# Performance work log

Hardware: AMD Instinct MI355X
Metric: run time of the kernel (lower is better)

The kernel has to match this reference:

```python
import jax, jax.numpy as jnp
import numpy as np

N = 50000
EPS = 1e-5


def gcn_conv(x, W, b, src, dst, n):
    # x: [n, Cin]; W: [Cin, Cout]; src/dst: [E+n] with self-loops included
    h = x @ W  # dense GEMM
    deg = jax.ops.segment_sum(jnp.ones_like(dst, dtype=h.dtype), dst, num_segments=n)
    dinv = jnp.where(deg > 0, jax.lax.rsqrt(deg), 0.0)
    norm = dinv[src] * dinv[dst]  # [E+n]
    msgs = h[src] * norm[:, None]  # gather + scale
    out = jax.ops.segment_sum(msgs, dst, num_segments=n)  # scatter-add
    return out + b


def batch_norm(x, gamma, beta, mean, var):
    return (x - mean) * jax.lax.rsqrt(var + EPS) * gamma + beta


def setup_inputs() -> dict:
    key = jax.random.key(0)
    ks = jax.random.split(key, 16)
    IN, H, OUT, E = 1280, 256, 500, 1600000
    x = jax.random.normal(ks[0], (N, IN), dtype=jnp.float32)
    edge_index = jax.random.randint(ks[1], (2, E), 0, N, dtype=jnp.int64)
    def lin(k, cin, cout):
        return jax.random.normal(k, (cin, cout), dtype=jnp.float32) / np.sqrt(cin)
    return {
        "x": x,
        "edge_index": edge_index,
        "W1": lin(ks[2], IN, H), "b1": jnp.zeros((H,), jnp.float32),
        "g1": jnp.ones((H,), jnp.float32), "be1": jnp.zeros((H,), jnp.float32),
        "m1": 0.1 * jax.random.normal(ks[3], (H,), jnp.float32),
        "v1": 0.5 + jax.random.uniform(ks[4], (H,), jnp.float32),
        "W2": lin(ks[5], H, H), "b2": jnp.zeros((H,), jnp.float32),
        "g2": jnp.ones((H,), jnp.float32), "be2": jnp.zeros((H,), jnp.float32),
        "m2": 0.1 * jax.random.normal(ks[6], (H,), jnp.float32),
        "v2": 0.5 + jax.random.uniform(ks[7], (H,), jnp.float32),
        "W3": lin(ks[8], H, OUT), "b3": jnp.zeros((OUT,), jnp.float32),
    }


def reference(x, edge_index, W1, b1, g1, be1, m1, v1, W2, b2, g2, be2, m2, v2, W3, b3):
    n = x.shape[0]
    loops = jnp.arange(n, dtype=edge_index.dtype)
    src = jnp.concatenate([edge_index[0], loops])
    dst = jnp.concatenate([edge_index[1], loops])
    h = gcn_conv(x, W1, b1, src, dst, n)
    h = jax.nn.relu(batch_norm(h, g1, be1, m1, v1))
    h = gcn_conv(h, W2, b2, src, dst, n)
    h = jax.nn.relu(batch_norm(h, g2, be2, m2, v2))
    return gcn_conv(h, W3, b3, src, dst, n)
```

## Files before the change

kernel.cpp:

```cpp
#include <hip/hip_runtime.h>
#include <hip/hip_bf16.h>
#include <stdint.h>

typedef __attribute__((ext_vector_type(4))) float f32x4;
typedef __attribute__((ext_vector_type(8))) short s16x8;
typedef __attribute__((ext_vector_type(4))) unsigned short u16x4;

#define EPSBN 1e-5f

__device__ __forceinline__ float bf2f(unsigned short u) {
  union { unsigned int i; float f; } w; w.i = ((unsigned int)u) << 16; return w.f;
}
__device__ __forceinline__ unsigned short f2bf(float f) {
  __hip_bfloat16 h = __float2bfloat16(f);
  unsigned short u; __builtin_memcpy(&u, &h, 2); return u;
}
__device__ __forceinline__ void gld_lds16(const unsigned short* g, unsigned short* l) {
  __builtin_amdgcn_global_load_lds(
      (__attribute__((address_space(1))) void*)(g),
      (__attribute__((address_space(3))) void*)(l), 16, 0, 0);
}

__global__ void k_init_deg(unsigned* deg, int n) {
  int i = blockIdx.x * 256 + threadIdx.x;
  if (i < n) deg[i] = 1u;
}
__global__ void k_count(const int* __restrict__ dst, unsigned* __restrict__ deg, int E) {
  int i = blockIdx.x * 256 + threadIdx.x;
  if (i < E) atomicAdd(&deg[dst[i]], 1u);
}
__global__ void k_dinv(const unsigned* __restrict__ deg, float* __restrict__ dinv, int n) {
  int i = blockIdx.x * 256 + threadIdx.x;
  if (i < n) dinv[i] = rsqrtf((float)deg[i]);
}
__global__ void k_bsum(const unsigned* __restrict__ deg, unsigned* __restrict__ bsum, int n) {
  __shared__ unsigned s[256];
  int t = threadIdx.x, i = blockIdx.x * 256 + t;
  s[t] = (i < n) ? deg[i] : 0u;
  __syncthreads();
  for (int st = 128; st > 0; st >>= 1) {
    if (t < st) s[t] += s[t + st];
    __syncthreads();
  }
  if (t == 0) bsum[blockIdx.x] = s[0];
}
__global__ void k_scan_top(const unsigned* __restrict__ bsum, unsigned* __restrict__ bpre,
                           int nb, unsigned* __restrict__ offs, int n) {
  __shared__ unsigned s[256];
  int t = threadIdx.x;
  unsigned v = (t < nb) ? bsum[t] : 0u;
  s[t] = v; __syncthreads();
  for (int d = 1; d < 256; d <<= 1) {
    unsigned a = (t >= d) ? s[t - d] : 0u;
    __syncthreads();
    s[t] += a;
    __syncthreads();
  }
  bpre[t] = s[t] - v;
  if (t == 255) offs[n] = s[255];
}
__global__ void k_scan_fin(const unsigned* __restrict__ deg, const unsigned* __restrict__ bpre,
                           unsigned* __restrict__ offs, unsigned* __restrict__ cur, int n) {
  __shared__ unsigned s[256];
  int t = threadIdx.x, i = blockIdx.x * 256 + t;
  unsigned v = (i < n) ? deg[i] : 0u;
  s[t] = v; __syncthreads();
  for (int d = 1; d < 256; d <<= 1) {
    unsigned a = (t >= d) ? s[t - d] : 0u;
    __syncthreads();
    s[t] += a;
    __syncthreads();
  }
  if (i < n) {
    unsigned o = bpre[blockIdx.x] + s[t] - v;
    offs[i] = o; cur[i] = o;
  }
}
__global__ void k_fill(const int* __restrict__ src, const int* __restrict__ dst,
                       unsigned* __restrict__ cur, int* __restrict__ adj, int E, int n) {
  int i = blockIdx.x * 256 + threadIdx.x;
  int s, d;
  if (i < E)          { s = src[i]; d = dst[i]; }
  else if (i < E + n) { s = d = i - E; }
  else return;
  unsigned p = atomicAdd(&cur[d], 1u);
  adj[p] = s;
}
#define SORT_CAP 96
__global__ __launch_bounds__(256) void k_sort(const unsigned* __restrict__ offs,
                                              int* __restrict__ adj, int nN) {
  __shared__ int buf[SORT_CAP * 256];
  int t = threadIdx.x;
  int v = blockIdx.x * 256 + t;
  if (v >= nN) return;
  unsigned b = offs[v], e = offs[v + 1];
  int len = (int)(e - b);
  if (len > SORT_CAP) return;
  for (int i = 0; i < len; ++i) buf[i * 256 + t] = adj[b + i];
  for (int i = 1; i < len; ++i) {
    int key = buf[i * 256 + t];
    int j = i - 1;
    while (j >= 0 && buf[j * 256 + t] > key) {
      buf[(j + 1) * 256 + t] = buf[j * 256 + t];
      --j;
    }
    buf[(j + 1) * 256 + t] = key;
  }
  for (int i = 0; i < len; ++i) adj[b + i] = buf[i * 256 + t];
}
__global__ __launch_bounds__(256) void k_edgew(const int* __restrict__ adj,
                                               const unsigned* __restrict__ offs,
                                               const float* __restrict__ dinv,
                                               int2* __restrict__ ew, int nN) {
  int wv = (blockIdx.x * 256 + threadIdx.x) >> 6;
  int lane = threadIdx.x & 63;
  if (wv >= nN) return;
  unsigned beg = offs[wv], end = offs[wv + 1];
  float dv = dinv[wv];
  for (unsigned e = beg + lane; e < end; e += 64) {
    int s = adj[e];
    ew[e] = make_int2(s, __float_as_int(dinv[s] * dv));
  }
}
__global__ void k_wt(const float* __restrict__ W, unsigned short* __restrict__ Wt,
                     int K, int N, int Npad) {
  int idx = blockIdx.x * 256 + threadIdx.x;
  if (idx >= Npad * K) return;
  int nn = idx / K, k = idx - nn * K;
  float v = (nn < N) ? W[(size_t)k * N + nn] : 0.f;
  Wt[idx] = f2bf(v);
}

#define BM 128
#define BN 128
#define BK 64

template<int CONVA, int OUTF32>
__global__ __launch_bounds__(256, 2) void k_gemm(
    const void* __restrict__ Aall, const unsigned short* __restrict__ Bt,
    void* __restrict__ Coutv, const float* __restrict__ bias,
    int M, int N, int K, int MT, int NT)
{
  __shared__ __align__(16) unsigned short As[BM * BK];
  __shared__ __align__(16) unsigned short Bs[BN * BK];

  int d = blockIdx.x;
  int xc = d & 7, sb = d >> 3;
  int nt = sb % NT, mt = (sb / NT) * 8 + xc;
  if (mt >= MT) return;
  int m0 = mt * BM, n0 = nt * BN;

  int tid = threadIdx.x, lane = tid & 63, wave = tid >> 6;
  int wm = wave >> 1, wn = wave & 1;
  int l15 = lane & 15, l4 = lane >> 4;

  f32x4 acc[4][4];
#pragma unroll
  for (int i = 0; i < 4; ++i)
#pragma unroll
    for (int j = 0; j < 4; ++j) acc[i][j] = 0.f;

  int srow[4], scg[4], sci[4];
#pragma unroll
  for (int i = 0; i < 4; ++i) {
    int ci = (wave + 4 * i) * 64 + lane;
    sci[i] = ci;
    srow[i] = ci >> 3;
    scg[i] = (ci & 7) ^ (srow[i] & 7);
  }
  const float* Af = (const float*)Aall;
  const unsigned short* Au = (const unsigned short*)Aall;

  int nk = K / BK;
  for (int kt = 0; kt < nk; ++kt) {
    __syncthreads();
#pragma unroll
    for (int i = 0; i < 4; ++i) {
      int gr = m0 + srow[i]; gr = gr < M ? gr : M - 1;
      if (CONVA) {
        const float* p = Af + (size_t)gr * K + kt * BK + scg[i] * 8;
        f32x4 f0 = *(const f32x4*)p;
        f32x4 f1 = *(const f32x4*)(p + 4);
        s16x8 pk;
        pk[0] = (short)f2bf(f0[0]); pk[1] = (short)f2bf(f0[1]);
        pk[2] = (short)f2bf(f0[2]); pk[3] = (short)f2bf(f0[3]);
        pk[4] = (short)f2bf(f1[0]); pk[5] = (short)f2bf(f1[1]);
        pk[6] = (short)f2bf(f1[2]); pk[7] = (short)f2bf(f1[3]);
        *(s16x8*)(As + sci[i] * 8) = pk;
      } else {
        gld_lds16(Au + (size_t)gr * K + kt * BK + scg[i] * 8, As + (wave + 4 * i) * 512);
      }
    }
#pragma unroll
    for (int i = 0; i < 4; ++i) {
      int gn = n0 + srow[i];
      gld_lds16(Bt + (size_t)gn * K + kt * BK + scg[i] * 8, Bs + (wave + 4 * i) * 512);
    }
    __syncthreads();

#pragma unroll
    for (int ks = 0; ks < 2; ++ks) {
      s16x8 af[4], bf[4];
#pragma unroll
      for (int f = 0; f < 4; ++f) {
        int r = wm * 64 + f * 16 + l15;
        int ca = (ks * 4 + l4) ^ (r & 7);
        af[f] = *(const s16x8*)(As + r * 64 + ca * 8);
        int nloc = wn * 64 + f * 16 + l15;
        int cb = (ks * 4 + l4) ^ (nloc & 7);
        bf[f] = *(const s16x8*)(Bs + nloc * 64 + cb * 8);
      }
#pragma unroll
      for (int fm = 0; fm < 4; ++fm)
#pragma unroll
        for (int fn = 0; fn < 4; ++fn)
          acc[fm][fn] = __builtin_amdgcn_mfma_f32_16x16x32_bf16(af[fm], bf[fn], acc[fm][fn], 0, 0, 0);
    }
  }

#pragma unroll
  for (int fm = 0; fm < 4; ++fm) {
#pragma unroll
    for (int fn = 0; fn < 4; ++fn) {
#pragma unroll
      for (int r = 0; r < 4; ++r) {
        int row = m0 + wm * 64 + fm * 16 + l4 * 4 + r;
        int col = n0 + wn * 64 + fn * 16 + l15;
        if (row < M && col < N) {
          if (OUTF32)
            ((float*)Coutv)[(size_t)row * N + col] = acc[fm][fn][r] + bias[col];
          else
            ((unsigned short*)Coutv)[(size_t)row * N + col] = f2bf(acc[fm][fn][r]);
        }
      }
    }
  }
}

__device__ __forceinline__ void accum4(float& a0, float& a1, float& a2, float& a3,
                                       u16x4 q, float w) {
  a0 += bf2f(q[0]) * w; a1 += bf2f(q[1]) * w;
  a2 += bf2f(q[2]) * w; a3 += bf2f(q[3]) * w;
}

template<int BNRELU, int BIAS>
__global__ __launch_bounds__(256) void k_agg(
    const unsigned short* __restrict__ h, const int2* __restrict__ ew,
    const unsigned* __restrict__ offs, const float* __restrict__ bias,
    const float* __restrict__ gam, const float* __restrict__ bet,
    const float* __restrict__ mea, const float* __restrict__ var,
    unsigned short* __restrict__ outp, int nN)
{
  const int C = 256;
  int wave = threadIdx.x >> 6, lane = threadIdx.x & 63;
  int v = blockIdx.x * 4 + wave;
  if (v >= nN) return;
  unsigned beg = offs[v], end = offs[v + 1];
  int len = (int)(end - beg);
  int ch0 = lane * 4;
  const unsigned short* hb = h + ch0;
  float a0 = 0, a1 = 0, a2 = 0, a3 = 0;

  for (int base = 0; base < len; base += 64) {
    int m = min(64, len - base);
    int2 myp = make_int2(0, 0);
    if (lane < m) myp = ew[beg + base + lane];
    int ng = (m + 3) >> 2;

    int sA0 = __shfl(myp.x, 0), sA1 = __shfl(myp.x, 1);
    int sA2 = __shfl(myp.x, 2), sA3 = __shfl(myp.x, 3);
    float wA0 = __int_as_float(__shfl(myp.y, 0));
    float wA1 = __int_as_float(__shfl(myp.y, 1));
    float wA2 = __int_as_float(__shfl(myp.y, 2));
    float wA3 = __int_as_float(__shfl(myp.y, 3));
    u16x4 qA0 = *(const u16x4*)(hb + (size_t)sA0 * C);
    u16x4 qA1 = *(const u16x4*)(hb + (size_t)sA1 * C);
    u16x4 qA2 = *(const u16x4*)(hb + (size_t)sA2 * C);
    u16x4 qA3 = *(const u16x4*)(hb + (size_t)sA3 * C);

    for (int g = 1; g < ng; ++g) {
      int b = g << 2;
      int sB0 = __shfl(myp.x, b + 0), sB1 = __shfl(myp.x, b + 1);
      int sB2 = __shfl(myp.x, b + 2), sB3 = __shfl(myp.x, b + 3);
      float wB0 = __int_as_float(__shfl(myp.y, b + 0));
      float wB1 = __int_as_float(__shfl(myp.y, b + 1));
      float wB2 = __int_as_float(__shfl(myp.y, b + 2));
      float wB3 = __int_as_float(__shfl(myp.y, b + 3));
      u16x4 qB0 = *(const u16x4*)(hb + (size_t)sB0 * C);
      u16x4 qB1 = *(const u16x4*)(hb + (size_t)sB1 * C);
      u16x4 qB2 = *(const u16x4*)(hb + (size_t)sB2 * C);
      u16x4 qB3 = *(const u16x4*)(hb + (size_t)sB3 * C);
      accum4(a0, a1, a2, a3, qA0, wA0);
      accum4(a0, a1, a2, a3, qA1, wA1);
      accum4(a0, a1, a2, a3, qA2, wA2);
      accum4(a0, a1, a2, a3, qA3, wA3);
      qA0 = qB0; wA0 = wB0; qA1 = qB1; wA1 = wB1;
      qA2 = qB2; wA2 = wB2; qA3 = qB3; wA3 = wB3;
    }
    accum4(a0, a1, a2, a3, qA0, wA0);
    accum4(a0, a1, a2, a3, qA1, wA1);
    accum4(a0, a1, a2, a3, qA2, wA2);
    accum4(a0, a1, a2, a3, qA3, wA3);
  }

  float va[4] = {a0, a1, a2, a3};
#pragma unroll
  for (int j = 0; j < 4; ++j) {
    int ch = ch0 + j;
    float val = va[j];
    if (BIAS) val += bias[ch];
    if (BNRELU) {
      val = (val - mea[ch]) * rsqrtf(var[ch] + EPSBN) * gam[ch] + bet[ch];
      val = fmaxf(val, 0.f);
    }
    outp[(size_t)v * C + ch] = f2bf(val);
  }
}

extern "C" void kernel_launch(void* const* d_in, const int* in_sizes, int n_in,
                              void* d_out, int out_size, void* d_ws, size_t ws_size,
                              hipStream_t stream) {
  const float* x   = (const float*)d_in[0];
  const int*   ei  = (const int*)d_in[1];
  const float* W1  = (const float*)d_in[2];
  const float* b1  = (const float*)d_in[3];
  const float* g1  = (const float*)d_in[4];
  const float* be1 = (const float*)d_in[5];
  const float* m1  = (const float*)d_in[6];
  const float* v1  = (const float*)d_in[7];
  const float* W2  = (const float*)d_in[8];
  const float* b2  = (const float*)d_in[9];
  const float* g2  = (const float*)d_in[10];
  const float* be2 = (const float*)d_in[11];
  const float* m2  = (const float*)d_in[12];
  const float* v2  = (const float*)d_in[13];
  const float* W3  = (const float*)d_in[14];
  const float* b3  = (const float*)d_in[15];

  const int IN = 1280, H = 256, OUT = 500, OUTP = 512;
  int E  = in_sizes[1] / 2;
  int nN = in_sizes[0] / IN;
  const int* srcI = ei;
  const int* dstI = ei + E;

  char* p = (char*)d_ws;
  auto carve = [&](size_t bytes) { char* r = p; p += (bytes + 511) & ~(size_t)511; return r; };
  unsigned short* Wt1 = (unsigned short*)carve((size_t)H * IN * 2);
  unsigned short* Wt2 = (unsigned short*)carve((size_t)H * H * 2);
  unsigned short* Wt3 = (unsigned short*)carve((size_t)OUTP * H * 2);
  unsigned* deg  = (unsigned*)carve((size_t)nN * 4);
  float*    dinv = (float*)carve((size_t)nN * 4);
  unsigned* offs = (unsigned*)carve((size_t)(nN + 1) * 4);
  unsigned* cur  = (unsigned*)carve((size_t)nN * 4);
  unsigned* bsum = (unsigned*)carve(256 * 4);
  unsigned* bpre = (unsigned*)carve(256 * 4);
  int*      adj  = (int*)carve((size_t)(E + nN) * 4);
  int2*     ew   = (int2*)carve((size_t)(E + nN) * 8);
  unsigned short* bufA = (unsigned short*)carve((size_t)nN * H * 2);
  unsigned short* bufB = (unsigned short*)carve((size_t)nN * H * 2);

  int NB = (nN + 255) / 256;
  k_init_deg<<<NB, 256, 0, stream>>>(deg, nN);
  k_count<<<(E + 255) / 256, 256, 0, stream>>>(dstI, deg, E);
  k_dinv<<<NB, 256, 0, stream>>>(deg, dinv, nN);
  k_bsum<<<NB, 256, 0, stream>>>(deg, bsum, nN);
  k_scan_top<<<1, 256, 0, stream>>>(bsum, bpre, NB, offs, nN);
  k_scan_fin<<<NB, 256, 0, stream>>>(deg, bpre, offs, cur, nN);
  k_fill<<<(E + nN + 255) / 256, 256, 0, stream>>>(srcI, dstI, cur, adj, E, nN);
  k_sort<<<NB, 256, 0, stream>>>(offs, adj, nN);
  k_edgew<<<(nN + 3) / 4, 256, 0, stream>>>(adj, offs, dinv, ew, nN);

  k_wt<<<(H * IN + 255) / 256, 256, 0, stream>>>(W1, Wt1, IN, H, H);
  k_wt<<<(H * H + 255) / 256, 256, 0, stream>>>(W2, Wt2, H, H, H);
  k_wt<<<(OUTP * H + 255) / 256, 256, 0, stream>>>(W3, Wt3, H, OUT, OUTP);

  int MT = (nN + BM - 1) / BM;
  int mg = (MT + 7) / 8;
  int nAgg = (nN + 3) / 4;

  k_gemm<1, 0><<<mg * 8 * 2, 256, 0, stream>>>(x, Wt1, bufA, nullptr, nN, H, IN, MT, 2);
  k_agg<1, 1><<<nAgg, 256, 0, stream>>>(bufA, ew, offs, b1, g1, be1, m1, v1, bufB, nN);
  k_gemm<0, 0><<<mg * 8 * 2, 256, 0, stream>>>(bufB, Wt2, bufA, nullptr, nN, H, H, MT, 2);
  k_agg<1, 1><<<nAgg, 256, 0, stream>>>(bufA, ew, offs, b2, g2, be2, m2, v2, bufB, nN);
  k_agg<0, 0><<<nAgg, 256, 0, stream>>>(bufB, ew, offs, nullptr, nullptr, nullptr, nullptr, nullptr, bufA, nN);
  k_gemm<0, 1><<<mg * 8 * 4, 256, 0, stream>>>(bufA, Wt3, d_out, b3, nN, OUT, H, MT, 4);
}
```

Measured before the change: 826.8 us.

## Fuse adjacency sort into edge-weight kernel, async-load fp32 A in first GEMM, widen aggregation prefetch

Replaces the per-thread insertion sort in shared memory plus the separate edge-weight pass with one wave-level bitonic sort over shuffles, which also writes the weights. Neighbour lists longer than 64 are left unsorted. Adds a dedicated first-layer GEMM that loads fp32 x straight into LDS with direct global-to-LDS loads and converts to bf16 on the fragment read, instead of converting in registers before storing to LDS. It also raises the occupancy hints on the GEMMs and doubles the aggregation gather batch from 4 to 8 neighbours to keep more loads in flight. The fp32 LDS tile doubles the A-tile shared-memory footprint, and the larger batch raises register pressure.

```diff
diff --git a/kernel.cpp b/kernel.cpp
--- a/kernel.cpp
+++ b/kernel.cpp
@@ -15,9 +15,9 @@
   __hip_bfloat16 h = __float2bfloat16(f);
   unsigned short u; __builtin_memcpy(&u, &h, 2); return u;
 }
-__device__ __forceinline__ void gld_lds16(const unsigned short* g, unsigned short* l) {
+__device__ __forceinline__ void gld_lds16(const void* g, void* l) {
   __builtin_amdgcn_global_load_lds(
-      (__attribute__((address_space(1))) void*)(g),
+      (const __attribute__((address_space(1))) void*)(g),
       (__attribute__((address_space(3))) void*)(l), 16, 0, 0);
 }
 
@@ -86,40 +86,34 @@
   unsigned p = atomicAdd(&cur[d], 1u);
   adj[p] = s;
 }
-#define SORT_CAP 96
-__global__ __launch_bounds__(256) void k_sort(const unsigned* __restrict__ offs,
-                                              int* __restrict__ adj, int nN) {
-  __shared__ int buf[SORT_CAP * 256];
-  int t = threadIdx.x;
-  int v = blockIdx.x * 256 + t;
-  if (v >= nN) return;
-  unsigned b = offs[v], e = offs[v + 1];
-  int len = (int)(e - b);
-  if (len > SORT_CAP) return;
-  for (int i = 0; i < len; ++i) buf[i * 256 + t] = adj[b + i];
-  for (int i = 1; i < len; ++i) {
-    int key = buf[i * 256 + t];
-    int j = i - 1;
-    while (j >= 0 && buf[j * 256 + t] > key) {
-      buf[(j + 1) * 256 + t] = buf[j * 256 + t];
-      --j;
-    }
-    buf[(j + 1) * 256 + t] = key;
-  }
-  for (int i = 0; i < len; ++i) adj[b + i] = buf[i * 256 + t];
-}
-__global__ __launch_bounds__(256) void k_edgew(const int* __restrict__ adj,
-                                               const unsigned* __restrict__ offs,
+__global__ __launch_bounds__(256) void k_sortw(const unsigned* __restrict__ offs,
+                                               const int* __restrict__ adj,
                                                const float* __restrict__ dinv,
                                                int2* __restrict__ ew, int nN) {
   int wv = (blockIdx.x * 256 + threadIdx.x) >> 6;
   int lane = threadIdx.x & 63;
   if (wv >= nN) return;
   unsigned beg = offs[wv], end = offs[wv + 1];
+  int len = (int)(end - beg);
   float dv = dinv[wv];
-  for (unsigned e = beg + lane; e < end; e += 64) {
-    int s = adj[e];
-    ew[e] = make_int2(s, __float_as_int(dinv[s] * dv));
+  if (len <= 64) {
+    int k = (lane < len) ? adj[beg + lane] : 0x7FFFFFFF;
+#pragma unroll
+    for (int size = 2; size <= 64; size <<= 1) {
+#pragma unroll
+      for (int stride = size >> 1; stride > 0; stride >>= 1) {
+        int other = __shfl_xor(k, stride);
+        bool up = (lane & size) == 0;
+        bool lower = (lane & stride) == 0;
+        k = (lower == up) ? min(k, other) : max(k, other);
+      }
+    }
+    if (lane < len) ew[beg + lane] = make_int2(k, __float_as_int(dinv[k] * dv));
+  } else {
+    for (unsigned e = beg + lane; e < end; e += 64) {
+      int s = adj[e];
+      ew[e] = make_int2(s, __float_as_int(dinv[s] * dv));
+    }
   }
 }
 __global__ void k_wt(const float* __restrict__ W, unsigned short* __restrict__ Wt,
@@ -135,9 +129,9 @@
 #define BN 128
 #define BK 64
 
-template<int CONVA, int OUTF32>
-__global__ __launch_bounds__(256, 2) void k_gemm(
-    const void* __restrict__ Aall, const unsigned short* __restrict__ Bt,
+template<int OUTF32>
+__global__ __launch_bounds__(256, 4) void k_gemm(
+    const unsigned short* __restrict__ Au, const unsigned short* __restrict__ Bt,
     void* __restrict__ Coutv, const float* __restrict__ bias,
     int M, int N, int K, int MT, int NT)
 {
@@ -160,16 +154,13 @@
 #pragma unroll
     for (int j = 0; j < 4; ++j) acc[i][j] = 0.f;
 
-  int srow[4], scg[4], sci[4];
+  int srow[4], scg[4];
 #pragma unroll
   for (int i = 0; i < 4; ++i) {
     int ci = (wave + 4 * i) * 64 + lane;
-    sci[i] = ci;
     srow[i] = ci >> 3;
     scg[i] = (ci & 7) ^ (srow[i] & 7);
   }
-  const float* Af = (const float*)Aall;
-  const unsigned short* Au = (const unsigned short*)Aall;
 
   int nk = K / BK;
   for (int kt = 0; kt < nk; ++kt) {
@@ -177,19 +168,7 @@
 #pragma unroll
     for (int i = 0; i < 4; ++i) {
       int gr = m0 + srow[i]; gr = gr < M ? gr : M - 1;
-      if (CONVA) {
-        const float* p = Af + (size_t)gr * K + kt * BK + scg[i] * 8;
-        f32x4 f0 = *(const f32x4*)p;
-        f32x4 f1 = *(const f32x4*)(p + 4);
-        s16x8 pk;
-        pk[0] = (short)f2bf(f0[0]); pk[1] = (short)f2bf(f0[1]);
-        pk[2] = (short)f2bf(f0[2]); pk[3] = (short)f2bf(f0[3]);
-        pk[4] = (short)f2bf(f1[0]); pk[5] = (short)f2bf(f1[1]);
-        pk[6] = (short)f2bf(f1[2]); pk[7] = (short)f2bf(f1[3]);
-        *(s16x8*)(As + sci[i] * 8) = pk;
-      } else {
-        gld_lds16(Au + (size_t)gr * K + kt * BK + scg[i] * 8, As + (wave + 4 * i) * 512);
-      }
+      gld_lds16(Au + (size_t)gr * K + kt * BK + scg[i] * 8, As + (wave + 4 * i) * 512);
     }
 #pragma unroll
     for (int i = 0; i < 4; ++i) {
@@ -232,6 +211,101 @@
           else
             ((unsigned short*)Coutv)[(size_t)row * N + col] = f2bf(acc[fm][fn][r]);
         }
+      }
+    }
+  }
+}
+
+__global__ __launch_bounds__(256, 3) void k_gemmF(
+    const float* __restrict__ Af, const unsigned short* __restrict__ Bt,
+    unsigned short* __restrict__ Cout, int M, int N, int K, int MT, int NT)
+{
+  __shared__ __align__(16) float As[BM * BK];
+  __shared__ __align__(16) unsigned short Bs[BN * BK];
+
+  int d = blockIdx.x;
+  int xc = d & 7, sb = d >> 3;
+  int nt = sb % NT, mt = (sb / NT) * 8 + xc;
+  if (mt >= MT) return;
+  int m0 = mt * BM, n0 = nt * BN;
+
+  int tid = threadIdx.x, lane = tid & 63, wave = tid >> 6;
+  int wm = wave >> 1, wn = wave & 1;
+  int l15 = lane & 15, l4 = lane >> 4;
+
+  f32x4 acc[4][4];
+#pragma unroll
+  for (int i = 0; i < 4; ++i)
+#pragma unroll
+    for (int j = 0; j < 4; ++j) acc[i][j] = 0.f;
+
+  int arow[8], acs[8];
+#pragma unroll
+  for (int i = 0; i < 8; ++i) {
+    int ci = (i * 4 + wave) * 64 + lane;
+    arow[i] = ci >> 4;
+    acs[i] = (ci & 15) ^ ((arow[i] & 7) << 1);
+  }
+  int brow[4], bcg[4];
+#pragma unroll
+  for (int i = 0; i < 4; ++i) {
+    int ci = (i * 4 + wave) * 64 + lane;
+    brow[i] = ci >> 3;
+    bcg[i] = (ci & 7) ^ (brow[i] & 7);
+  }
+
+  int nk = K / BK;
+  for (int kt = 0; kt < nk; ++kt) {
+    __syncthreads();
+#pragma unroll
+    for (int i = 0; i < 8; ++i) {
+      int gr = m0 + arow[i]; gr = gr < M ? gr : M - 1;
+      gld_lds16(Af + (size_t)gr * K + kt * BK + acs[i] * 4, As + (i * 4 + wave) * 256);
+    }
+#pragma unroll
+    for (int i = 0; i < 4; ++i) {
+      int gn = n0 + brow[i];
+      gld_lds16(Bt + (size_t)gn * K + kt * BK + bcg[i] * 8, Bs + (i * 4 + wave) * 512);
+    }
+    __syncthreads();
+
+#pragma unroll
+    for (int ks = 0; ks < 2; ++ks) {
+      s16x8 af[4], bf[4];
+#pragma unroll
+      for (int f = 0; f < 4; ++f) {
+        int r = wm * 64 + f * 16 + l15;
+        int c0 = (2 * (ks * 4 + l4)) ^ ((r & 7) << 1);
+        f32x4 a0 = *(const f32x4*)(As + r * 64 + c0 * 4);
+        f32x4 a1 = *(const f32x4*)(As + r * 64 + c0 * 4 + 4);
+        s16x8 pk;
+        pk[0] = (short)f2bf(a0[0]); pk[1] = (short)f2bf(a0[1]);
+        pk[2] = (short)f2bf(a0[2]); pk[3] = (short)f2bf(a0[3]);
+        pk[4] = (short)f2bf(a1[0]); pk[5] = (short)f2bf(a1[1]);
+        pk[6] = (short)f2bf(a1[2]); pk[7] = (short)f2bf(a1[3]);
+        af[f] = pk;
+        int nloc = wn * 64 + f * 16 + l15;
+        int cb = (ks * 4 + l4) ^ (nloc & 7);
+        bf[f] = *(const s16x8*)(Bs + nloc * 64 + cb * 8);
+      }
+#pragma unroll
+      for (int fm = 0; fm < 4; ++fm)
+#pragma unroll
+        for (int fn = 0; fn < 4; ++fn)
+          acc[fm][fn] = __builtin_amdgcn_mfma_f32_16x16x32_bf16(af[fm], bf[fn], acc[fm][fn], 0, 0, 0);
+    }
+  }
+
+#pragma unroll
+  for (int fm = 0; fm < 4; ++fm) {
+#pragma unroll
+    for (int fn = 0; fn < 4; ++fn) {
+#pragma unroll
+      for (int r = 0; r < 4; ++r) {
+        int row = m0 + wm * 64 + fm * 16 + l4 * 4 + r;
+        int col = n0 + wn * 64 + fn * 16 + l15;
+        if (row < M && col < N)
+          Cout[(size_t)row * N + col] = f2bf(acc[fm][fn][r]);
       }
     }
   }
@@ -265,42 +339,31 @@
     int m = min(64, len - base);
     int2 myp = make_int2(0, 0);
     if (lane < m) myp = ew[beg + base + lane];
-    int ng = (m + 3) >> 2;
-
-    int sA0 = __shfl(myp.x, 0), sA1 = __shfl(myp.x, 1);
-    int sA2 = __shfl(myp.x, 2), sA3 = __shfl(myp.x, 3);
-    float wA0 = __int_as_float(__shfl(myp.y, 0));
-    float wA1 = __int_as_float(__shfl(myp.y, 1));
-    float wA2 = __int_as_float(__shfl(myp.y, 2));
-    float wA3 = __int_as_float(__shfl(myp.y, 3));
-    u16x4 qA0 = *(const u16x4*)(hb + (size_t)sA0 * C);
-    u16x4 qA1 = *(const u16x4*)(hb + (size_t)sA1 * C);
-    u16x4 qA2 = *(const u16x4*)(hb + (size_t)sA2 * C);
-    u16x4 qA3 = *(const u16x4*)(hb + (size_t)sA3 * C);
-
+    int ng = (m + 7) >> 3;
+
+    u16x4 q[8]; float w[8];
+#pragma unroll
+    for (int r = 0; r < 8; ++r) {
+      int s = __shfl(myp.x, r);
+      w[r] = __int_as_float(__shfl(myp.y, r));
+      q[r] = *(const u16x4*)(hb + (size_t)s * C);
+    }
     for (int g = 1; g < ng; ++g) {
-      int b = g << 2;
-      int sB0 = __shfl(myp.x, b + 0), sB1 = __shfl(myp.x, b + 1);
-      int sB2 = __shfl(myp.x, b + 2), sB3 = __shfl(myp.x, b + 3);
-      float wB0 = __int_as_float(__shfl(myp.y, b + 0));
-      float wB1 = __int_as_float(__shfl(myp.y, b + 1));
-      float wB2 = __int_as_float(__shfl(myp.y, b + 2));
-      float wB3 = __int_as_float(__shfl(myp.y, b + 3));
-      u16x4 qB0 = *(const u16x4*)(hb + (size_t)sB0 * C);
-      u16x4 qB1 = *(const u16x4*)(hb + (size_t)sB1 * C);
-      u16x4 qB2 = *(const u16x4*)(hb + (size_t)sB2 * C);
-      u16x4 qB3 = *(const u16x4*)(hb + (size_t)sB3 * C);
-      accum4(a0, a1, a2, a3, qA0, wA0);
-      accum4(a0, a1, a2, a3, qA1, wA1);
-      accum4(a0, a1, a2, a3, qA2, wA2);
-      accum4(a0, a1, a2, a3, qA3, wA3);
-      qA0 = qB0; wA0 = wB0; qA1 = qB1; wA1 = wB1;
-      qA2 = qB2; wA2 = wB2; qA3 = qB3; wA3 = wB3;
-    }
-    accum4(a0, a1, a2, a3, qA0, wA0);
-    accum4(a0, a1, a2, a3, qA1, wA1);
-    accum4(a0, a1, a2, a3, qA2, wA2);
-    accum4(a0, a1, a2, a3, qA3, wA3);
+      u16x4 q2[8]; float w2[8];
+#pragma unroll
+      for (int r = 0; r < 8; ++r) {
+        int b = g * 8 + r;
+        int s = __shfl(myp.x, b);
+        w2[r] = __int_as_float(__shfl(myp.y, b));
+        q2[r] = *(const u16x4*)(hb + (size_t)s * C);
+      }
+#pragma unroll
+      for (int r = 0; r < 8; ++r) accum4(a0, a1, a2, a3, q[r], w[r]);
+#pragma unroll
+      for (int r = 0; r < 8; ++r) { q[r] = q2[r]; w[r] = w2[r]; }
+    }
+#pragma unroll
+    for (int r = 0; r < 8; ++r) accum4(a0, a1, a2, a3, q[r], w[r]);
   }
 
   float va[4] = {a0, a1, a2, a3};
@@ -367,8 +430,7 @@
   k_scan_top<<<1, 256, 0, stream>>>(bsum, bpre, NB, offs, nN);
   k_scan_fin<<<NB, 256, 0, stream>>>(deg, bpre, offs, cur, nN);
   k_fill<<<(E + nN + 255) / 256, 256, 0, stream>>>(srcI, dstI, cur, adj, E, nN);
-  k_sort<<<NB, 256, 0, stream>>>(offs, adj, nN);
-  k_edgew<<<(nN + 3) / 4, 256, 0, stream>>>(adj, offs, dinv, ew, nN);
+  k_sortw<<<(nN + 3) / 4, 256, 0, stream>>>(offs, adj, dinv, ew, nN);
 
   k_wt<<<(H * IN + 255) / 256, 256, 0, stream>>>(W1, Wt1, IN, H, H);
   k_wt<<<(H * H + 255) / 256, 256, 0, stream>>>(W2, Wt2, H, H, H);
@@ -378,10 +440,10 @@
   int mg = (MT + 7) / 8;
   int nAgg = (nN + 3) / 4;
 
-  k_gemm<1, 0><<<mg * 8 * 2, 256, 0, stream>>>(x, Wt1, bufA, nullptr, nN, H, IN, MT, 2);
+  k_gemmF<<<mg * 8 * 2, 256, 0, stream>>>(x, Wt1, bufA, nN, H, IN, MT, 2);
   k_agg<1, 1><<<nAgg, 256, 0, stream>>>(bufA, ew, offs, b1, g1, be1, m1, v1, bufB, nN);
-  k_gemm<0, 0><<<mg * 8 * 2, 256, 0, stream>>>(bufB, Wt2, bufA, nullptr, nN, H, H, MT, 2);
+  k_gemm<0><<<mg * 8 * 2, 256, 0, stream>>>(bufB, Wt2, bufA, nullptr, nN, H, H, MT, 2);
   k_agg<1, 1><<<nAgg, 256, 0, stream>>>(bufA, ew, offs, b2, g2, be2, m2, v2, bufB, nN);
   k_agg<0, 0><<<nAgg, 256, 0, stream>>>(bufB, ew, offs, nullptr, nullptr, nullptr, nullptr, nullptr, bufA, nN);
-  k_gemm<0, 1><<<mg * 8 * 4, 256, 0, stream>>>(bufA, Wt3, d_out, b3, nN, OUT, H, MT, 4);
-}
+  k_gemm<1><<<mg * 8 * 4, 256, 0, stream>>>(bufA, Wt3, d_out, b3, nN, OUT, H, MT, 4);
+}
```

Measured after the change: 701.9 us. -15.1%, faster.
